# Optimization experiments

Hardware: AMD Instinct MI355X
Metric: run time of the kernel (lower is better)

The kernel has to match this reference:

```python
import jax, jax.numpy as jnp
import numpy as np

B, HT_, WT_, DM, C = 32, 32, 32, 768, 64  # batch, token grid, token dim, hough channels
THETA_RES, RHO_RES = 3, 1


def hough_transform(rows, cols, theta_res, rho_res):
    """Precompute binary vote matrix [rows*cols, n_rho*n_theta] (HT-LCNN style)."""
    theta = np.linspace(0.0, 180.0, int(np.ceil(180.0 / theta_res)) + 1)[:-1]
    w = theta.size                                # n_theta
    diag = np.sqrt((rows - 1) ** 2 + (cols - 1) ** 2)
    q = int(np.ceil(diag / rho_res))
    nrho = 2 * q + 1                              # n_rho
    cos_t, sin_t = np.cos(np.deg2rad(theta)), np.sin(np.deg2rad(theta))
    ii, jj = np.meshgrid(np.arange(rows), np.arange(cols), indexing='ij')
    xc = jj - cols / 2.0                          # centered pixel coords
    yc = rows / 2.0 - ii
    rho = xc[..., None] * cos_t + yc[..., None] * sin_t   # [rows, cols, w]
    ridx = np.round(rho / rho_res).astype(np.int64) + q
    tidx = np.broadcast_to(np.arange(w), ridx.shape)
    flat = (ridx * w + tidx).reshape(rows * cols, w)      # bin = rho_idx*w + theta_idx
    vote = np.zeros((rows * cols, nrho * w), dtype=np.float32)
    vote[np.arange(rows * cols)[:, None], flat] = 1.0
    return vote, nrho, w


def setup_inputs() -> dict:
    key = jax.random.key(0)
    ks = jax.random.split(key, 8)
    vote_np, n_rho, n_theta = hough_transform(HT_, WT_, THETA_RES, RHO_RES)
    ch = C // 2
    s = lambda n: 1.0 / np.sqrt(n)
    return dict(
        tokens=jax.random.normal(ks[0], (B, HT_ * WT_, DM), jnp.float32),
        vote=jnp.asarray(vote_np),                                    # [N, HR]
        Wt_in=jax.random.normal(ks[1], (C, DM), jnp.float32) * s(DM),   # to_feats 1x1
        bt_in=jnp.zeros((C,), jnp.float32),
        W1=jax.random.normal(ks[2], (ch, C), jnp.float32) * s(C),       # conv1 1x1 (no bias)
        W2=jax.random.normal(ks[3], (ch, ch, 9, 1), jnp.float32) * s(ch * 9),  # (9,1) conv on hough map
        W3=jax.random.normal(ks[4], (C, ch), jnp.float32) * s(ch),      # conv3 1x1 (no bias)
        Wt_out=jax.random.normal(ks[5], (DM, C), jnp.float32) * s(C),   # from_feats 1x1
        bt_out=jnp.zeros((DM,), jnp.float32),
        n_rho=n_rho,
        n_theta=n_theta,
    )


def reference(tokens, vote, Wt_in, bt_in, W1, W2, W3, Wt_out, bt_out, n_rho, n_theta):
    # tokens: [B, N, D]; vote: [N, HR] with HR = n_rho * n_theta.
    # 1x1 convs over the token grid are position-independent -> plain matmuls on [B, N, *].
    norm = jnp.clip(vote.sum(0), 1.0)                       # [HR] HT vote-count normalizer
    feat = tokens @ Wt_in.T + bt_in                         # [B, N, C]   (to_feats)
    y = jax.nn.relu(feat @ W1.T)                            # [B, N, ch]  (conv1 + relu)
    # HT: relu (idempotent here) + vote gather as dense matmul, normalized per hough bin
    ht = jnp.einsum('bnc,nh->bch', y, vote) / norm          # [B, ch, HR]
    bb, ch, hr = ht.shape
    ht = ht.reshape(bb, ch, n_rho, n_theta)                 # [B, ch, n_rho, n_theta]
    ht = jax.lax.conv_general_dilated(                      # (9,1) conv along rho, pad 4
        ht, W2, (1, 1), ((4, 4), (0, 0)),
        dimension_numbers=('NCHW', 'OIHW', 'NCHW'))
    # IHT: relu + transposed vote scatter, normalized by n_theta
    iht = jnp.einsum('bch,nh->bnc', jax.nn.relu(ht.reshape(bb, ch, hr)), vote) / n_theta
    z = iht @ W3.T                                          # [B, N, C]   (conv3)
    out = (feat + z) @ Wt_out.T + bt_out                    # residual + from_feats -> [B, N, D]
    return out
```

## Files before the change

kernel.cpp:

```cpp
#include <hip/hip_runtime.h>
#include <math.h>

#define NB    32
#define NTOK  1024
#define DMODEL 768
#define CF    64
#define CHH   32
#define NRHO  89
#define NTH   60
#define HRB   (NRHO*NTH)

typedef short bf16x8 __attribute__((ext_vector_type(8)));
typedef float f32x4  __attribute__((ext_vector_type(4)));
typedef unsigned int uint;
typedef unsigned short ushort;
typedef unsigned char uchar;

__device__ __forceinline__ ushort f2bf(float f) {
    uint u = __float_as_uint(f);
    return (ushort)((u + 0x7FFF + ((u >> 16) & 1)) >> 16);
}
__device__ __forceinline__ float bf2f(ushort u) {
    return __uint_as_float(((uint)u) << 16);
}

#define GLDS16(gp, lp) __builtin_amdgcn_global_load_lds( \
    (const __attribute__((address_space(1))) unsigned int*)(gp), \
    (__attribute__((address_space(3))) unsigned int*)(lp), 16, 0, 0)

__global__ __launch_bounds__(256) void k0_prep(
    int* __restrict__ perm, int* __restrict__ rowptr, uchar* __restrict__ rho8,
    const float* __restrict__ Wt_in, const float* __restrict__ bt_in,
    const float* __restrict__ W1, short* __restrict__ wcat,
    float* __restrict__ bcat,
    const float* __restrict__ Wt_out, const float* __restrict__ W2,
    short* __restrict__ wout, short* __restrict__ w2t) {
    __shared__ int rho_n[NTOK];
    __shared__ int cnt2[64 * 90];
    __shared__ int tot[96];
    __shared__ int base[96];
    __shared__ float w1row[64];
    const int tid = threadIdx.x;
    const int blk = blockIdx.x;

    if (blk < 60) {
        const int t = blk;
        const double rad = ((double)(t * 3)) * (M_PI / 180.0);
        const double ct = cos(rad), st = sin(rad);
        for (int n = tid; n < NTOK; n += 256) {
            int i = n >> 5, j = n & 31;
            double rho = (double)(j - 16) * ct + (double)(16 - i) * st;
            int ridx = (int)rint(rho) + 44;
            rho_n[n] = ridx;
            rho8[t * NTOK + n] = (uchar)ridx;
        }
        for (int i = tid; i < 64 * 90; i += 256) cnt2[i] = 0;
        __syncthreads();
        for (int n = tid; n < NTOK; n += 256)
            atomicAdd(&cnt2[(n >> 4) * 90 + rho_n[n]], 1);
        __syncthreads();
        if (tid < NRHO) {
            int s = 0;
            for (int c = 0; c < 64; ++c) {
                int v = cnt2[c * 90 + tid];
                cnt2[c * 90 + tid] = s;
                s += v;
            }
            tot[tid] = s;
        }
        __syncthreads();
        if (tid == 0) {
            int s = 0;
            for (int r = 0; r < NRHO; ++r) { base[r] = s; s += tot[r]; }
            base[NRHO] = s;
        }
        __syncthreads();
        if (tid < NRHO + 1) rowptr[t * 90 + tid] = base[tid];
        if (tid < 64) {
            const int c = tid;
            #pragma unroll
            for (int j = 0; j < 16; ++j) {
                int n = c * 16 + j;
                int r = rho_n[n];
                int cur = cnt2[c * 90 + r];
                cnt2[c * 90 + r] = cur + 1;
                perm[t * NTOK + base[r] + cur] = n;
            }
        }
    } else if (blk < 156) {
        const int c = blk - 60;
        if (c >= 64)
            for (int j = tid; j < 64; j += 256) w1row[j] = W1[(c - 64) * 64 + j];
        __syncthreads();
        for (int k = tid; k < DMODEL; k += 256) {
            float v;
            if (c < 64) v = Wt_in[c * DMODEL + k];
            else {
                v = 0.0f;
                for (int j = 0; j < 64; ++j) v += w1row[j] * Wt_in[j * DMODEL + k];
            }
            int kt = k >> 6, kk = k & 63;
            wcat[(((kt << 3) + (kk >> 3)) * 96 + c) * 8 + (k & 7)] = (short)f2bf(v);
        }
        if (tid == 0) {
            float bv;
            if (c < 64) bv = bt_in[c];
            else {
                bv = 0.0f;
                for (int j = 0; j < 64; ++j) bv += W1[(c - 64) * 64 + j] * bt_in[j];
            }
            bcat[c] = bv;
        }
    } else {
        int idx = (blk - 156) * 256 + tid;
        if (idx < 6144) {
            int d = idx >> 3, kg = idx & 7;
            float4 a = *(const float4*)&Wt_out[d * 64 + kg * 8];
            float4 b = *(const float4*)&Wt_out[d * 64 + kg * 8 + 4];
            uint p0 = (uint)f2bf(a.x) | ((uint)f2bf(a.y) << 16);
            uint p1 = (uint)f2bf(a.z) | ((uint)f2bf(a.w) << 16);
            uint p2 = (uint)f2bf(b.x) | ((uint)f2bf(b.y) << 16);
            uint p3 = (uint)f2bf(b.z) | ((uint)f2bf(b.w) << 16);
            uint4 v = make_uint4(p0, p1, p2, p3);
            *(uint4*)&wout[(((d >> 7) * 8 + kg) * 128 + (d & 127)) * 8] = v;
        } else if (idx < 6144 + 9216) {
            int q = idx - 6144;
            int e = q & 7, ln = (q >> 3) & 63, wm = (q >> 9) & 1, k = q >> 10;
            int o = wm * 16 + (ln & 15), i = ((ln >> 4) << 3) + e;
            w2t[q] = (short)f2bf(W2[(o * 32 + i) * 9 + k]);
        }
    }
}

__global__ __launch_bounds__(256) void k1_mfma(
    const float* __restrict__ tokens, const short* __restrict__ wcat,
    const float* __restrict__ bcat, ushort* __restrict__ featb,
    ushort* __restrict__ ybb) {
    __shared__ __align__(16) short Asm[2][4096];
    __shared__ __align__(16) short Bsm[2][6144];

    const int tid = threadIdx.x;
    const int lane = tid & 63, wave = tid >> 6;
    const int wm = wave >> 1, wn = wave & 1;
    const int row0 = blockIdx.x * 64;
    const int sm = tid >> 2, sq = tid & 3;

    const float* arow = tokens + (size_t)(row0 + sm) * DMODEL;

    f32x4 acc[2][3] = {};
    float4 ta[4];

    #pragma unroll
    for (int p = 0; p < 4; ++p)
        ta[p] = *(const float4*)&arow[(sq + 4 * p) * 4];
    for (int ch = tid; ch < 768; ch += 256)
        GLDS16((const char*)wcat + ch * 16, (char*)Bsm[0] + ch * 16);
    #pragma unroll
    for (int p = 0; p < 4; ++p) {
        int q = sq + 4 * p, kg = q >> 1, half = q & 1;
        uint lo = (uint)f2bf(ta[p].x) | ((uint)f2bf(ta[p].y) << 16);
        uint hi = (uint)f2bf(ta[p].z) | ((uint)f2bf(ta[p].w) << 16);
        *(uint2*)((char*)Asm[0] + (kg * 64 + sm) * 16 + half * 8) = make_uint2(lo, hi);
    }
    __syncthreads();

    int cur = 0;
    for (int kt = 0; kt < 12; ++kt) {
        if (kt < 11) {
            const float* src = arow + (kt + 1) * 64;
            #pragma unroll
            for (int p = 0; p < 4; ++p)
                ta[p] = *(const float4*)&src[(sq + 4 * p) * 4];
            const char* bsrc = (const char*)wcat + (size_t)(kt + 1) * 12288;
            for (int ch = tid; ch < 768; ch += 256)
                GLDS16(bsrc + ch * 16, (char*)Bsm[cur ^ 1] + ch * 16);
        }
        const bf16x8* Ap = (const bf16x8*)Asm[cur];
        const bf16x8* Bp = (const bf16x8*)Bsm[cur];
        #pragma unroll
        for (int ks = 0; ks < 2; ++ks) {
            int kg = (lane >> 4) + ks * 4;
            bf16x8 av[2], bv[3];
            #pragma unroll
            for (int i = 0; i < 2; ++i)
                av[i] = Ap[kg * 64 + wm * 32 + i * 16 + (lane & 15)];
            #pragma unroll
            for (int j = 0; j < 3; ++j)
                bv[j] = Bp[kg * 96 + wn * 48 + j * 16 + (lane & 15)];
            #pragma unroll
            for (int i = 0; i < 2; ++i)
                #pragma unroll
                for (int j = 0; j < 3; ++j)
                    acc[i][j] = __builtin_amdgcn_mfma_f32_16x16x32_bf16(
                        av[i], bv[j], acc[i][j], 0, 0, 0);
        }
        if (kt < 11) {
            #pragma unroll
            for (int p = 0; p < 4; ++p) {
                int q = sq + 4 * p, kg = q >> 1, half = q & 1;
                uint lo = (uint)f2bf(ta[p].x) | ((uint)f2bf(ta[p].y) << 16);
                uint hi = (uint)f2bf(ta[p].z) | ((uint)f2bf(ta[p].w) << 16);
                *(uint2*)((char*)Asm[cur ^ 1] + (kg * 64 + sm) * 16 + half * 8) =
                    make_uint2(lo, hi);
            }
        }
        __syncthreads();
        cur ^= 1;
    }

    float bb[3];
    #pragma unroll
    for (int j = 0; j < 3; ++j) bb[j] = bcat[wn * 48 + j * 16 + (lane & 15)];
    #pragma unroll
    for (int i = 0; i < 2; ++i) {
        #pragma unroll
        for (int j = 0; j < 3; ++j) {
            int c = wn * 48 + j * 16 + (lane & 15);
            #pragma unroll
            for (int r = 0; r < 4; ++r) {
                int m = row0 + wm * 32 + i * 16 + ((lane >> 4) << 2) + r;
                float v = acc[i][j][r] + bb[j];
                if (c < 64) featb[(size_t)m * CF + c] = f2bf(v);
                else        ybb[(size_t)m * CHH + (c - 64)] = f2bf(fmaxf(v, 0.0f));
            }
        }
    }
}

__global__ __launch_bounds__(256) void k23_ht_conv(
    const ushort* __restrict__ ybb, const int* __restrict__ perm,
    const int* __restrict__ rowptr, const short* __restrict__ w2t,
    ushort* __restrict__ htcT) {
    __shared__ int pperm[NTOK];
    __shared__ int prow[90];
    __shared__ __align__(16) short insp[104 * 40];
    __shared__ ushort outts[NRHO * 36];

    const int tid = threadIdx.x;
    const int lane = tid & 63, wave = tid >> 6;
    const int wm = wave >> 1, wn = wave & 1;
    const int b = blockIdx.x / NTH, t = blockIdx.x % NTH;

    bf16x8 av[9];
    #pragma unroll
    for (int k = 0; k < 9; ++k)
        av[k] = *(const bf16x8*)&w2t[(((k * 2 + wm) * 64) + lane) * 8];

    for (int i = tid; i < NTOK; i += 256) pperm[i] = perm[t * NTOK + i];
    for (int i = tid; i < 90; i += 256) prow[i] = rowptr[t * 90 + i];
    for (int i = tid; i < 104 * 40 / 2; i += 256) ((uint*)insp)[i] = 0;
    __syncthreads();

    {
        const int c0 = (tid & 7) * 4, g = tid >> 3;
        const ushort* yp = ybb + (size_t)b * NTOK * CHH + c0;
        for (int rho = g; rho < NRHO; rho += 32) {
            int p0 = prow[rho], p1 = prow[rho + 1];
            float s0 = 0.0f, s1 = 0.0f, s2 = 0.0f, s3 = 0.0f;
            for (int k = p0; k < p1; ++k) {
                int n = pperm[k];
                ushort4 v = *(const ushort4*)&yp[n * CHH];
                s0 += bf2f(v.x); s1 += bf2f(v.y); s2 += bf2f(v.z); s3 += bf2f(v.w);
            }
            float iv = 1.0f / fmaxf((float)(p1 - p0), 1.0f);
            uint q0 = (uint)f2bf(s0 * iv) | ((uint)f2bf(s1 * iv) << 16);
            uint q1 = (uint)f2bf(s2 * iv) | ((uint)f2bf(s3 * iv) << 16);
            *(uint2*)&insp[(rho + 4) * 40 + c0] = make_uint2(q0, q1);
        }
    }
    __syncthreads();

    f32x4 acc[3] = {};
    #pragma unroll
    for (int f = 0; f < 3; ++f) {
        int Rn = wn * 48 + f * 16 + (lane & 15);
        #pragma unroll
        for (int k = 0; k < 9; ++k) {
            bf16x8 bv = *(const bf16x8*)&insp[(Rn + k) * 40 + ((lane >> 4) << 3)];
            acc[f] = __builtin_amdgcn_mfma_f32_16x16x32_bf16(av[k], bv, acc[f], 0, 0, 0);
        }
    }
    #pragma unroll
    for (int f = 0; f < 3; ++f) {
        int r = wn * 48 + f * 16 + (lane & 15);
        if (r < NRHO) {
            #pragma unroll
            for (int reg = 0; reg < 4; ++reg) {
                int o = wm * 16 + ((lane >> 4) << 2) + reg;
                outts[r * 36 + o] = f2bf(fmaxf(acc[f][reg], 0.0f));
            }
        }
    }
    __syncthreads();

    {
        ushort* dst = htcT + (size_t)(b * NTH + t) * (NRHO * CHH);
        for (int idx = tid; idx < NRHO * 8; idx += 256) {
            int r = idx >> 3, cq = (idx & 7) * 4;
            ushort4 v;
            v.x = outts[r * 36 + cq];     v.y = outts[r * 36 + cq + 1];
            v.z = outts[r * 36 + cq + 2]; v.w = outts[r * 36 + cq + 3];
            *(ushort4*)&dst[r * CHH + cq] = v;
        }
    }
}

__global__ __launch_bounds__(256) void k4_iht_z(
    const ushort* __restrict__ htcT, const uchar* __restrict__ rho8,
    const float* __restrict__ W3, const ushort* __restrict__ featb,
    short* __restrict__ g) {
    __shared__ float w3t[32 * 64];
    __shared__ uchar lrho[NTH * 32];
    __shared__ float ihts[32 * 32];
    __shared__ __align__(16) ushort gs16[32 * 72];
    const int tid = threadIdx.x;
    const int b = blockIdx.x >> 5;
    const int n0 = (blockIdx.x & 31) * 32;

    for (int idx = tid; idx < 2048; idx += 256) {
        int c = idx >> 6, j = idx & 63;
        w3t[idx] = W3[j * 32 + c];
    }
    for (int idx = tid; idx < NTH * 32; idx += 256) {
        int t = idx >> 5, tok = idx & 31;
        lrho[t * 32 + tok] = rho8[t * NTOK + n0 + tok];
    }
    __syncthreads();

    {
        const int c0 = (tid & 7) * 4, tok = tid >> 3;
        const ushort* hb = htcT + (size_t)b * NTH * NRHO * CHH + c0;
        float s0 = 0.0f, s1 = 0.0f, s2 = 0.0f, s3 = 0.0f;
        #pragma unroll 10
        for (int t = 0; t < NTH; ++t) {
            int r = lrho[t * 32 + tok];
            ushort4 v = *(const ushort4*)&hb[(t * NRHO + r) * CHH];
            s0 += bf2f(v.x); s1 += bf2f(v.y); s2 += bf2f(v.z); s3 += bf2f(v.w);
        }
        float4 rr;
        rr.x = s0 * (1.0f / 60.0f); rr.y = s1 * (1.0f / 60.0f);
        rr.z = s2 * (1.0f / 60.0f); rr.w = s3 * (1.0f / 60.0f);
        *(float4*)&ihts[tok * 32 + c0] = rr;
    }
    __syncthreads();

    const int j = tid & 63, nb = tid >> 6;
    for (int nn = nb; nn < 32; nn += 4) {
        float z = 0.0f;
        #pragma unroll 8
        for (int cc = 0; cc < 32; ++cc) z += ihts[nn * 32 + cc] * w3t[cc * 64 + j];
        float v = bf2f(featb[((size_t)b * NTOK + n0 + nn) * CF + j]) + z;
        gs16[nn * 72 + j] = f2bf(v);
    }
    __syncthreads();

    {
        int nnl = tid >> 3, kg = tid & 7;
        bf16x8 frag = *(const bf16x8*)&gs16[nnl * 72 + kg * 8];
        int m = b * NTOK + n0 + nnl;
        int mt = m >> 7, mloc = m & 127;
        *(bf16x8*)&g[((mt * 8 + kg) * 128 + mloc) * 8] = frag;
    }
}

__global__ __launch_bounds__(256) void k5_mfma(
    const short* __restrict__ g, const short* __restrict__ wout,
    const float* __restrict__ bt_out, float* __restrict__ out) {
    __shared__ __align__(16) short Asm[8192];
    __shared__ __align__(16) short Bsm[8192];
    const int tid = threadIdx.x;
    const int lane = tid & 63, wave = tid >> 6;
    const int wm = wave >> 1, wn = wave & 1;
    const int mb = blockIdx.x / 6, db = blockIdx.x % 6;

    for (int ch = tid; ch < 1024; ch += 256) {
        GLDS16((const char*)g + (size_t)mb * 16384 + ch * 16, (char*)Asm + ch * 16);
        GLDS16((const char*)wout + (size_t)db * 16384 + ch * 16, (char*)Bsm + ch * 16);
    }
    __syncthreads();

    f32x4 acc[4][4] = {};
    const bf16x8* Ap = (const bf16x8*)Asm;
    const bf16x8* Bp = (const bf16x8*)Bsm;
    #pragma unroll
    for (int ks = 0; ks < 2; ++ks) {
        int kg = (lane >> 4) + ks * 4;
        bf16x8 av[4], bv[4];
        #pragma unroll
        for (int i = 0; i < 4; ++i)
            av[i] = Ap[kg * 128 + wm * 64 + i * 16 + (lane & 15)];
        #pragma unroll
        for (int j = 0; j < 4; ++j)
            bv[j] = Bp[kg * 128 + wn * 64 + j * 16 + (lane & 15)];
        #pragma unroll
        for (int i = 0; i < 4; ++i)
            #pragma unroll
            for (int j = 0; j < 4; ++j)
                acc[i][j] = __builtin_amdgcn_mfma_f32_16x16x32_bf16(
                    av[i], bv[j], acc[i][j], 0, 0, 0);
    }

    const int d0 = db * 128 + wn * 64 + (lane & 15);
    float bb[4];
    #pragma unroll
    for (int j = 0; j < 4; ++j) bb[j] = bt_out[d0 + j * 16];
    const int mrow = mb * 128 + wm * 64 + ((lane >> 4) << 2);
    #pragma unroll
    for (int i = 0; i < 4; ++i)
        #pragma unroll
        for (int r = 0; r < 4; ++r)
            #pragma unroll
            for (int j = 0; j < 4; ++j)
                out[(size_t)(mrow + i * 16 + r) * DMODEL + d0 + j * 16] =
                    acc[i][j][r] + bb[j];
}

extern "C" void kernel_launch(void* const* d_in, const int* in_sizes, int n_in,
                              void* d_out, int out_size, void* d_ws, size_t ws_size,
                              hipStream_t stream) {
    const float* tokens = (const float*)d_in[0];
    const float* Wt_in  = (const float*)d_in[2];
    const float* bt_in  = (const float*)d_in[3];
    const float* W1     = (const float*)d_in[4];
    const float* W2     = (const float*)d_in[5];
    const float* W3     = (const float*)d_in[6];
    const float* Wt_out = (const float*)d_in[7];
    const float* bt_out = (const float*)d_in[8];
    float* out = (float*)d_out;

    char* w = (char*)d_ws;
    int*    perm   = (int*)(w);
    int*    rowptr = (int*)(w + 245760);
    uchar*  rho8   = (uchar*)(w + 267360);
    short*  wcat   = (short*)(w + 328800);
    float*  bcat   = (float*)(w + 476256);
    short*  wout   = (short*)(w + 476640);
    short*  w2t    = (short*)(w + 574944);
    ushort* featb  = (ushort*)(w + 593376);
    ushort* ybb    = (ushort*)(w + 4787680);
    short*  g      = (short*)(w + 6884832);
    ushort* htcT   = (ushort*)(w + 11079136);

    k0_prep<<<216, 256, 0, stream>>>(perm, rowptr, rho8, Wt_in, bt_in, W1,
                                     wcat, bcat, Wt_out, W2, wout, w2t);
    k1_mfma<<<NB * NTOK / 64, 256, 0, stream>>>(tokens, wcat, bcat, featb, ybb);
    k23_ht_conv<<<NB * NTH, 256, 0, stream>>>(ybb, perm, rowptr, w2t, htcT);
    k4_iht_z<<<NB * (NTOK / 32), 256, 0, stream>>>(htcT, rho8, W3, featb, g);
    k5_mfma<<<(NB * NTOK / 128) * (DMODEL / 128), 256, 0, stream>>>(g, wout, bt_out, out);
}
```

Measured before the change: 106.5 us.

## Fuse IHT/conv3 stage with output projection and use packed bf16 conversions

Merges the inverse-Hough plus conv3 kernel with the final from_feats GEMM into one 512-thread kernel. The residual tile now stays in LDS instead of round-tripping through the g buffer in global memory, and the kernel loops over six output column blocks with double-buffered weight loads. It also replaces manual float-to-bf16 rounding with the packed v_cvt_pk_bf16_f32 instruction, stages k1's epilogue through LDS for vectorized stores, and widens the IHT gather to 16-byte loads. The trade-off is a grid of only 256 large blocks with about 80KB of LDS each, which lowers occupancy and parallelism for the output GEMM and serializes its column blocks inside each block.

Result: faster. 101.0 us (-5.2%).

```diff
diff --git a/kernel.cpp b/kernel.cpp
--- a/kernel.cpp
+++ b/kernel.cpp
@@ -22,6 +22,11 @@
 }
 __device__ __forceinline__ float bf2f(ushort u) {
     return __uint_as_float(((uint)u) << 16);
+}
+__device__ __forceinline__ uint cvtpk(float lo, float hi) {
+    uint r;
+    asm("v_cvt_pk_bf16_f32 %0, %1, %2" : "=v"(r) : "v"(lo), "v"(hi));
+    return r;
 }
 
 #define GLDS16(gp, lp) __builtin_amdgcn_global_load_lds( \
@@ -117,11 +122,8 @@
             int d = idx >> 3, kg = idx & 7;
             float4 a = *(const float4*)&Wt_out[d * 64 + kg * 8];
             float4 b = *(const float4*)&Wt_out[d * 64 + kg * 8 + 4];
-            uint p0 = (uint)f2bf(a.x) | ((uint)f2bf(a.y) << 16);
-            uint p1 = (uint)f2bf(a.z) | ((uint)f2bf(a.w) << 16);
-            uint p2 = (uint)f2bf(b.x) | ((uint)f2bf(b.y) << 16);
-            uint p3 = (uint)f2bf(b.z) | ((uint)f2bf(b.w) << 16);
-            uint4 v = make_uint4(p0, p1, p2, p3);
+            uint4 v = make_uint4(cvtpk(a.x, a.y), cvtpk(a.z, a.w),
+                                 cvtpk(b.x, b.y), cvtpk(b.z, b.w));
             *(uint4*)&wout[(((d >> 7) * 8 + kg) * 128 + (d & 127)) * 8] = v;
         } else if (idx < 6144 + 9216) {
             int q = idx - 6144;
@@ -158,8 +160,8 @@
     #pragma unroll
     for (int p = 0; p < 4; ++p) {
         int q = sq + 4 * p, kg = q >> 1, half = q & 1;
-        uint lo = (uint)f2bf(ta[p].x) | ((uint)f2bf(ta[p].y) << 16);
-        uint hi = (uint)f2bf(ta[p].z) | ((uint)f2bf(ta[p].w) << 16);
+        uint lo = cvtpk(ta[p].x, ta[p].y);
+        uint hi = cvtpk(ta[p].z, ta[p].w);
         *(uint2*)((char*)Asm[0] + (kg * 64 + sm) * 16 + half * 8) = make_uint2(lo, hi);
     }
     __syncthreads();
@@ -198,8 +200,8 @@
             #pragma unroll
             for (int p = 0; p < 4; ++p) {
                 int q = sq + 4 * p, kg = q >> 1, half = q & 1;
-                uint lo = (uint)f2bf(ta[p].x) | ((uint)f2bf(ta[p].y) << 16);
-                uint hi = (uint)f2bf(ta[p].z) | ((uint)f2bf(ta[p].w) << 16);
+                uint lo = cvtpk(ta[p].x, ta[p].y);
+                uint hi = cvtpk(ta[p].z, ta[p].w);
                 *(uint2*)((char*)Asm[cur ^ 1] + (kg * 64 + sm) * 16 + half * 8) =
                     make_uint2(lo, hi);
             }
@@ -208,6 +210,8 @@
         cur ^= 1;
     }
 
+    ushort* fs = (ushort*)Asm[0];
+    ushort* ys = (ushort*)Asm[1];
     float bb[3];
     #pragma unroll
     for (int j = 0; j < 3; ++j) bb[j] = bcat[wn * 48 + j * 16 + (lane & 15)];
@@ -216,14 +220,23 @@
         #pragma unroll
         for (int j = 0; j < 3; ++j) {
             int c = wn * 48 + j * 16 + (lane & 15);
+            int mlb = wm * 32 + i * 16 + ((lane >> 4) << 2);
             #pragma unroll
             for (int r = 0; r < 4; ++r) {
-                int m = row0 + wm * 32 + i * 16 + ((lane >> 4) << 2) + r;
                 float v = acc[i][j][r] + bb[j];
-                if (c < 64) featb[(size_t)m * CF + c] = f2bf(v);
-                else        ybb[(size_t)m * CHH + (c - 64)] = f2bf(fmaxf(v, 0.0f));
-            }
-        }
+                if (c < 64) fs[(mlb + r) * 64 + c] = f2bf(v);
+                else        ys[(mlb + r) * 32 + (c - 64)] = f2bf(fmaxf(v, 0.0f));
+            }
+        }
+    }
+    __syncthreads();
+    for (int idx = tid; idx < 512; idx += 256) {
+        int ml = idx >> 3, cq = (idx & 7) * 8;
+        *(uint4*)&featb[(size_t)(row0 + ml) * CF + cq] = *(const uint4*)&fs[ml * 64 + cq];
+    }
+    {
+        int ml = tid >> 2, cq = (tid & 3) * 8;
+        *(uint4*)&ybb[(size_t)(row0 + ml) * CHH + cq] = *(const uint4*)&ys[ml * 32 + cq];
     }
 }
 
@@ -234,7 +247,7 @@
     __shared__ int pperm[NTOK];
     __shared__ int prow[90];
     __shared__ __align__(16) short insp[104 * 40];
-    __shared__ ushort outts[NRHO * 36];
+    __shared__ uint outtu[NRHO * 18];
 
     const int tid = threadIdx.x;
     const int lane = tid & 63, wave = tid >> 6;
@@ -263,9 +276,8 @@
                 s0 += bf2f(v.x); s1 += bf2f(v.y); s2 += bf2f(v.z); s3 += bf2f(v.w);
             }
             float iv = 1.0f / fmaxf((float)(p1 - p0), 1.0f);
-            uint q0 = (uint)f2bf(s0 * iv) | ((uint)f2bf(s1 * iv) << 16);
-            uint q1 = (uint)f2bf(s2 * iv) | ((uint)f2bf(s3 * iv) << 16);
-            *(uint2*)&insp[(rho + 4) * 40 + c0] = make_uint2(q0, q1);
+            *(uint2*)&insp[(rho + 4) * 40 + c0] =
+                make_uint2(cvtpk(s0 * iv, s1 * iv), cvtpk(s2 * iv, s3 * iv));
         }
     }
     __syncthreads();
@@ -284,11 +296,9 @@
     for (int f = 0; f < 3; ++f) {
         int r = wn * 48 + f * 16 + (lane & 15);
         if (r < NRHO) {
-            #pragma unroll
-            for (int reg = 0; reg < 4; ++reg) {
-                int o = wm * 16 + ((lane >> 4) << 2) + reg;
-                outts[r * 36 + o] = f2bf(fmaxf(acc[f][reg], 0.0f));
-            }
+            int ob = wm * 8 + ((lane >> 4) << 1);
+            outtu[r * 18 + ob]     = cvtpk(fmaxf(acc[f][0], 0.0f), fmaxf(acc[f][1], 0.0f));
+            outtu[r * 18 + ob + 1] = cvtpk(fmaxf(acc[f][2], 0.0f), fmaxf(acc[f][3], 0.0f));
         }
     }
     __syncthreads();
@@ -296,123 +306,122 @@
     {
         ushort* dst = htcT + (size_t)(b * NTH + t) * (NRHO * CHH);
         for (int idx = tid; idx < NRHO * 8; idx += 256) {
-            int r = idx >> 3, cq = (idx & 7) * 4;
-            ushort4 v;
-            v.x = outts[r * 36 + cq];     v.y = outts[r * 36 + cq + 1];
-            v.z = outts[r * 36 + cq + 2]; v.w = outts[r * 36 + cq + 3];
-            *(ushort4*)&dst[r * CHH + cq] = v;
-        }
-    }
-}
-
-__global__ __launch_bounds__(256) void k4_iht_z(
+            int r = idx >> 3, q = idx & 7;
+            uint2 v;
+            v.x = outtu[r * 18 + q * 2];
+            v.y = outtu[r * 18 + q * 2 + 1];
+            *(uint2*)&dst[r * CHH + q * 4] = v;
+        }
+    }
+}
+
+__global__ __launch_bounds__(512) void k45_iht_out(
     const ushort* __restrict__ htcT, const uchar* __restrict__ rho8,
     const float* __restrict__ W3, const ushort* __restrict__ featb,
-    short* __restrict__ g) {
-    __shared__ float w3t[32 * 64];
-    __shared__ uchar lrho[NTH * 32];
-    __shared__ float ihts[32 * 32];
-    __shared__ __align__(16) ushort gs16[32 * 72];
-    const int tid = threadIdx.x;
-    const int b = blockIdx.x >> 5;
-    const int n0 = (blockIdx.x & 31) * 32;
-
-    for (int idx = tid; idx < 2048; idx += 256) {
-        int c = idx >> 6, j = idx & 63;
-        w3t[idx] = W3[j * 32 + c];
-    }
-    for (int idx = tid; idx < NTH * 32; idx += 256) {
-        int t = idx >> 5, tok = idx & 31;
-        lrho[t * 32 + tok] = rho8[t * NTOK + n0 + tok];
-    }
-    __syncthreads();
-
-    {
-        const int c0 = (tid & 7) * 4, tok = tid >> 3;
-        const ushort* hb = htcT + (size_t)b * NTH * NRHO * CHH + c0;
-        float s0 = 0.0f, s1 = 0.0f, s2 = 0.0f, s3 = 0.0f;
-        #pragma unroll 10
-        for (int t = 0; t < NTH; ++t) {
-            int r = lrho[t * 32 + tok];
-            ushort4 v = *(const ushort4*)&hb[(t * NRHO + r) * CHH];
-            s0 += bf2f(v.x); s1 += bf2f(v.y); s2 += bf2f(v.z); s3 += bf2f(v.w);
-        }
-        float4 rr;
-        rr.x = s0 * (1.0f / 60.0f); rr.y = s1 * (1.0f / 60.0f);
-        rr.z = s2 * (1.0f / 60.0f); rr.w = s3 * (1.0f / 60.0f);
-        *(float4*)&ihts[tok * 32 + c0] = rr;
-    }
-    __syncthreads();
-
-    const int j = tid & 63, nb = tid >> 6;
-    for (int nn = nb; nn < 32; nn += 4) {
-        float z = 0.0f;
-        #pragma unroll 8
-        for (int cc = 0; cc < 32; ++cc) z += ihts[nn * 32 + cc] * w3t[cc * 64 + j];
-        float v = bf2f(featb[((size_t)b * NTOK + n0 + nn) * CF + j]) + z;
-        gs16[nn * 72 + j] = f2bf(v);
-    }
-    __syncthreads();
-
-    {
-        int nnl = tid >> 3, kg = tid & 7;
-        bf16x8 frag = *(const bf16x8*)&gs16[nnl * 72 + kg * 8];
-        int m = b * NTOK + n0 + nnl;
-        int mt = m >> 7, mloc = m & 127;
-        *(bf16x8*)&g[((mt * 8 + kg) * 128 + mloc) * 8] = frag;
-    }
-}
-
-__global__ __launch_bounds__(256) void k5_mfma(
-    const short* __restrict__ g, const short* __restrict__ wout,
-    const float* __restrict__ bt_out, float* __restrict__ out) {
-    __shared__ __align__(16) short Asm[8192];
-    __shared__ __align__(16) short Bsm[8192];
+    const short* __restrict__ wout, const float* __restrict__ bt_out,
+    float* __restrict__ out) {
+    __shared__ __align__(16) char smem[81408];
+    short* Alds = (short*)smem;
+    short* Blds = (short*)(smem + 16384);
+    float* w3t  = (float*)(smem + 49152);
+    uchar* lrho = (uchar*)(smem + 57344);
+    float* ihts = (float*)(smem + 65024);
+
     const int tid = threadIdx.x;
     const int lane = tid & 63, wave = tid >> 6;
     const int wm = wave >> 1, wn = wave & 1;
-    const int mb = blockIdx.x / 6, db = blockIdx.x % 6;
-
-    for (int ch = tid; ch < 1024; ch += 256) {
-        GLDS16((const char*)g + (size_t)mb * 16384 + ch * 16, (char*)Asm + ch * 16);
-        GLDS16((const char*)wout + (size_t)db * 16384 + ch * 16, (char*)Bsm + ch * 16);
-    }
-    __syncthreads();
-
-    f32x4 acc[4][4] = {};
-    const bf16x8* Ap = (const bf16x8*)Asm;
-    const bf16x8* Bp = (const bf16x8*)Bsm;
-    #pragma unroll
-    for (int ks = 0; ks < 2; ++ks) {
-        int kg = (lane >> 4) + ks * 4;
-        bf16x8 av[4], bv[4];
-        #pragma unroll
-        for (int i = 0; i < 4; ++i)
-            av[i] = Ap[kg * 128 + wm * 64 + i * 16 + (lane & 15)];
-        #pragma unroll
-        for (int j = 0; j < 4; ++j)
-            bv[j] = Bp[kg * 128 + wn * 64 + j * 16 + (lane & 15)];
-        #pragma unroll
-        for (int i = 0; i < 4; ++i)
-            #pragma unroll
-            for (int j = 0; j < 4; ++j)
-                acc[i][j] = __builtin_amdgcn_mfma_f32_16x16x32_bf16(
-                    av[i], bv[j], acc[i][j], 0, 0, 0);
-    }
-
-    const int d0 = db * 128 + wn * 64 + (lane & 15);
-    float bb[4];
-    #pragma unroll
-    for (int j = 0; j < 4; ++j) bb[j] = bt_out[d0 + j * 16];
-    const int mrow = mb * 128 + wm * 64 + ((lane >> 4) << 2);
-    #pragma unroll
-    for (int i = 0; i < 4; ++i)
-        #pragma unroll
-        for (int r = 0; r < 4; ++r)
-            #pragma unroll
-            for (int j = 0; j < 4; ++j)
-                out[(size_t)(mrow + i * 16 + r) * DMODEL + d0 + j * 16] =
-                    acc[i][j][r] + bb[j];
+    const int b = blockIdx.x >> 3;
+    const int n0 = (blockIdx.x & 7) * 128;
+
+    for (int ch = tid; ch < 1024; ch += 512)
+        GLDS16((const char*)wout + ch * 16, (char*)Blds + ch * 16);
+
+    for (int idx = tid; idx < 2048; idx += 512) {
+        int c = idx >> 6, j = idx & 63;
+        w3t[idx] = W3[j * 32 + c];
+    }
+    for (int idx = tid; idx < NTH * 128; idx += 512)
+        lrho[idx] = rho8[(idx >> 7) * NTOK + n0 + (idx & 127)];
+    __syncthreads();
+
+    {
+        const int c0 = (tid & 3) * 8, tok = tid >> 2;
+        const ushort* hb = htcT + (size_t)b * NTH * NRHO * CHH + c0;
+        float s[8] = {};
+        #pragma unroll 6
+        for (int t = 0; t < NTH; ++t) {
+            int r = lrho[t * 128 + tok];
+            uint4 v = *(const uint4*)&hb[(size_t)(t * NRHO + r) * CHH];
+            s[0] += bf2f((ushort)(v.x & 0xffff)); s[1] += bf2f((ushort)(v.x >> 16));
+            s[2] += bf2f((ushort)(v.y & 0xffff)); s[3] += bf2f((ushort)(v.y >> 16));
+            s[4] += bf2f((ushort)(v.z & 0xffff)); s[5] += bf2f((ushort)(v.z >> 16));
+            s[6] += bf2f((ushort)(v.w & 0xffff)); s[7] += bf2f((ushort)(v.w >> 16));
+        }
+        float4 r0, r1;
+        r0.x = s[0] * (1.0f / 60.0f); r0.y = s[1] * (1.0f / 60.0f);
+        r0.z = s[2] * (1.0f / 60.0f); r0.w = s[3] * (1.0f / 60.0f);
+        r1.x = s[4] * (1.0f / 60.0f); r1.y = s[5] * (1.0f / 60.0f);
+        r1.z = s[6] * (1.0f / 60.0f); r1.w = s[7] * (1.0f / 60.0f);
+        *(float4*)&ihts[tok * 32 + c0] = r0;
+        *(float4*)&ihts[tok * 32 + c0 + 4] = r1;
+    }
+    __syncthreads();
+
+    {
+        const int j = tid & 63, nb = tid >> 6;
+        ushort* Au = (ushort*)Alds;
+        for (int nn = nb; nn < 128; nn += 8) {
+            float z = 0.0f;
+            #pragma unroll 8
+            for (int cc = 0; cc < 32; ++cc) z += ihts[nn * 32 + cc] * w3t[cc * 64 + j];
+            float v = bf2f(featb[((size_t)b * NTOK + n0 + nn) * CF + j]) + z;
+            Au[((j >> 3) * 128 + nn) * 8 + (j & 7)] = f2bf(v);
+        }
+    }
+    __syncthreads();
+
+    const bf16x8* Ap = (const bf16x8*)Alds;
+    for (int db = 0; db < 6; ++db) {
+        if (db < 5) {
+            const char* src = (const char*)wout + (size_t)(db + 1) * 16384;
+            char* dst = (char*)Blds + ((db + 1) & 1) * 16384;
+            for (int ch = tid; ch < 1024; ch += 512)
+                GLDS16(src + ch * 16, dst + ch * 16);
+        }
+        const bf16x8* Bp = (const bf16x8*)((const char*)Blds + (db & 1) * 16384);
+        f32x4 acc[2][4] = {};
+        #pragma unroll
+        for (int ks = 0; ks < 2; ++ks) {
+            int kg = (lane >> 4) + ks * 4;
+            bf16x8 avv[2], bvv[4];
+            #pragma unroll
+            for (int i = 0; i < 2; ++i)
+                avv[i] = Ap[kg * 128 + wm * 32 + i * 16 + (lane & 15)];
+            #pragma unroll
+            for (int jf = 0; jf < 4; ++jf)
+                bvv[jf] = Bp[kg * 128 + wn * 64 + jf * 16 + (lane & 15)];
+            #pragma unroll
+            for (int i = 0; i < 2; ++i)
+                #pragma unroll
+                for (int jf = 0; jf < 4; ++jf)
+                    acc[i][jf] = __builtin_amdgcn_mfma_f32_16x16x32_bf16(
+                        avv[i], bvv[jf], acc[i][jf], 0, 0, 0);
+        }
+        const int d0 = db * 128 + wn * 64 + (lane & 15);
+        float bb[4];
+        #pragma unroll
+        for (int jf = 0; jf < 4; ++jf) bb[jf] = bt_out[d0 + jf * 16];
+        const int mrow = blockIdx.x * 128 + wm * 32 + ((lane >> 4) << 2);
+        #pragma unroll
+        for (int i = 0; i < 2; ++i)
+            #pragma unroll
+            for (int r = 0; r < 4; ++r)
+                #pragma unroll
+                for (int jf = 0; jf < 4; ++jf)
+                    out[(size_t)(mrow + i * 16 + r) * DMODEL + d0 + jf * 16] =
+                        acc[i][jf][r] + bb[jf];
+        __syncthreads();
+    }
 }
 
 extern "C" void kernel_launch(void* const* d_in, const int* in_sizes, int n_in,
@@ -438,13 +447,12 @@
     short*  w2t    = (short*)(w + 574944);
     ushort* featb  = (ushort*)(w + 593376);
     ushort* ybb    = (ushort*)(w + 4787680);
-    short*  g      = (short*)(w + 6884832);
-    ushort* htcT   = (ushort*)(w + 11079136);
+    ushort* htcT   = (ushort*)(w + 6884832);
 
     k0_prep<<<216, 256, 0, stream>>>(perm, rowptr, rho8, Wt_in, bt_in, W1,
                                      wcat, bcat, Wt_out, W2, wout, w2t);
     k1_mfma<<<NB * NTOK / 64, 256, 0, stream>>>(tokens, wcat, bcat, featb, ybb);
     k23_ht_conv<<<NB * NTH, 256, 0, stream>>>(ybb, perm, rowptr, w2t, htcT);
-    k4_iht_z<<<NB * (NTOK / 32), 256, 0, stream>>>(htcT, rho8, W3, featb, g);
-    k5_mfma<<<(NB * NTOK / 128) * (DMODEL / 128), 256, 0, stream>>>(g, wout, bt_out, out);
-}
+    k45_iht_out<<<NB * (NTOK / 128), 512, 0, stream>>>(htcT, rho8, W3, featb,
+                                                       wout, bt_out, out);
+}
```
